# Kernel tuning notes

Measured on AMD Instinct MI355X. Metric: run time of the kernel, lower is better.

## Reference

```python
import jax, jax.numpy as jnp
import numpy as np

B, S, D, H = 4, 1024, 1024, 16
DK = D // H


def _linear_params(key, scale):
    kw, kb = jax.random.split(key)
    W = jax.random.normal(kw, (D, D), dtype=jnp.float32) * scale
    b = jax.random.normal(kb, (D,), dtype=jnp.float32) * 0.01
    return W, b


def setup_inputs() -> dict:
    key = jax.random.key(0)
    ks = jax.random.split(key, 12)
    scale = 1.0 / np.sqrt(D)
    inp = {
        "query": jax.random.normal(ks[0], (B, S, D), dtype=jnp.float32),
        "key": jax.random.normal(ks[1], (B, S, D), dtype=jnp.float32),
        "value": jax.random.normal(ks[2], (B, S, D), dtype=jnp.float32),
        "time_k": jax.random.normal(ks[3], (B, S, D), dtype=jnp.float32),
        "time_v": jax.random.normal(ks[4], (B, S, D), dtype=jnp.float32),
        "mask": jnp.zeros((B, 1, S, S), dtype=jnp.float32),
    }
    names = ["Wq", "bq", "Wk", "bk", "Wv", "bv", "Wtk", "btk", "Wtv", "btv", "Wm", "bm"]
    for i in range(6):
        W, b = _linear_params(ks[5 + i], scale)
        inp[names[2 * i]] = W
        inp[names[2 * i + 1]] = b
    return inp


def _split_heads(x):
    # [B,S,D] -> [B,H,S,DK]
    b, s, _ = x.shape
    return x.reshape(b, s, H, DK).transpose(0, 2, 1, 3)


def reference(query, key, value, time_k, time_v, mask,
              Wq, bq, Wk, bk, Wv, bv, Wtk, btk, Wtv, btv, Wm, bm):
    q = _split_heads(query @ Wq + bq)
    k = _split_heads(key @ Wk + bk)
    v = _split_heads(value @ Wv + bv)
    t_k = _split_heads(time_k @ Wtk + btk)
    t_v = _split_heads(time_v @ Wtv + btv)

    # scores[b,h,i,j] = q_i . k_j + t_k_i . q_j  (note second term uses q on the key axis)
    scores = jnp.einsum("bhid,bhjd->bhij", q, k) + jnp.einsum("bhid,bhjd->bhij", t_k, q)
    # module divides by sqrt(d_model) (query.size(-1)), not sqrt(d_k)
    scores = scores / jnp.sqrt(jnp.float32(D)) + mask
    probs = jax.nn.softmax(scores, axis=-1)

    # dropout is identity (p=0 / eval); squeeze(-2) is a no-op for S>1
    context = jnp.einsum("bhij,bhjd->bhid", probs, v) + jnp.einsum("bhij,bhjd->bhid", probs, t_v)
    x = context.transpose(0, 2, 1, 3).reshape(query.shape[0], -1, D)
    return x @ Wm + bm
```

## Files before the change

### kernel.cpp

```cpp
#include <hip/hip_runtime.h>
#include <hip/hip_bf16.h>
#include <cstdint>
#include <cstddef>

typedef __bf16 bf16;
typedef bf16 bf16x8 __attribute__((ext_vector_type(8)));
typedef bf16 bf16x4 __attribute__((ext_vector_type(4)));
typedef float f32x4 __attribute__((ext_vector_type(4)));
typedef unsigned int u32;

#define DEV static __device__ __forceinline__

DEV f32x4 mfma16(bf16x8 a, bf16x8 b, f32x4 c) {
    return __builtin_amdgcn_mfma_f32_16x16x32_bf16(a, b, c, 0, 0, 0);
}

DEV f32x4 shflx4(f32x4 v, int m) {
    f32x4 r;
    for (int i = 0; i < 4; ++i) r[i] = __shfl_xor(v[i], m, 64);
    return r;
}

DEV bf16x8 cvt8(const float* p) {
    float4 f0 = *(const float4*)p;
    float4 f1 = *(const float4*)(p + 4);
    bf16x8 v;
    v[0] = (bf16)f0.x; v[1] = (bf16)f0.y; v[2] = (bf16)f0.z; v[3] = (bf16)f0.w;
    v[4] = (bf16)f1.x; v[5] = (bf16)f1.y; v[6] = (bf16)f1.z; v[7] = (bf16)f1.w;
    return v;
}

DEV void glo(const bf16* g, bf16* l) {
    __builtin_amdgcn_global_load_lds(
        (const __attribute__((address_space(1))) u32*)g,
        (__attribute__((address_space(3))) u32*)l,
        16, 0, 0);
}


struct PrepArgs {
    const float* w[6];
    const float* act[5];
    bf16* wt;
    bf16* actbf[5];
};

__global__ __launch_bounds__(256) void prep_kernel(PrepArgs p)
{
    const int z = blockIdx.z;
    const int t = threadIdx.x;
    if (z < 6) {
        __shared__ bf16 tile[64][72];
        const float* src = p.w[z];
        bf16* out = p.wt + (size_t)z * 1024 * 1024;
        const int r = t >> 3, c8 = (t & 7) * 8;
        const int row0 = blockIdx.y * 64, col0 = blockIdx.x * 64;
        *(bf16x8*)&tile[r][c8]      = cvt8(&src[(size_t)(row0 + r) * 1024 + col0 + c8]);
        *(bf16x8*)&tile[r + 32][c8] = cvt8(&src[(size_t)(row0 + r + 32) * 1024 + col0 + c8]);
        __syncthreads();
        for (int half = 0; half < 2; ++half) {
            int rr = r + half * 32;
            bf16x8 v;
            for (int j = 0; j < 8; ++j) v[j] = tile[c8 + j][rr];
            *(bf16x8*)&out[(size_t)(col0 + rr) * 1024 + row0 + c8] = v;
        }
    } else {
        const float* src = p.act[z - 6];
        bf16* dst = p.actbf[z - 6];
        const size_t chunk = (size_t)(blockIdx.y * 16 + blockIdx.x) * 16384;
        for (int c = 0; c < 8; ++c) {
            const size_t off = chunk + (size_t)c * 2048 + (size_t)t * 8;
            *(bf16x8*)&dst[off] = cvt8(&src[off]);
        }
    }
}

__global__ __launch_bounds__(256) void maskprep_kernel(
    const float* __restrict__ mask, bf16* __restrict__ maskR)
{
    const int jt = blockIdx.x, it = blockIdx.y, b = blockIdx.z;
    __shared__ bf16 Mt[128 * 72];
    const int t = threadIdx.x, lane = t & 63, w = t >> 6;
    const int ln = lane & 15, qd = lane >> 4;
    {
        const int il = t >> 1, jh = (t & 1) * 32;
        const float* src = &mask[((size_t)b * 1024 + it * 128 + il) * 1024 + jt * 64 + jh];
        *(bf16x8*)&Mt[il * 72 + jh]      = cvt8(src);
        *(bf16x8*)&Mt[il * 72 + jh + 8]  = cvt8(src + 8);
        *(bf16x8*)&Mt[il * 72 + jh + 16] = cvt8(src + 16);
        *(bf16x8*)&Mt[il * 72 + jh + 24] = cvt8(src + 24);
    }
    __syncthreads();
    bf16 m[32];
    for (int si = 0; si < 2; ++si)
        for (int jc = 0; jc < 4; ++jc)
            for (int r = 0; r < 4; ++r) {
                const int il = w * 32 + si * 16 + qd * 4 + r;
                const int jl = jc * 16 + ln;
                m[(si * 4 + jc) * 4 + r] = Mt[il * 72 + jl];
            }
    bf16* dst = &maskR[((((size_t)b * 8 + it) * 16 + jt) * 256 + t) * 32];
    for (int c = 0; c < 4; ++c)
        *(bf16x8*)&dst[c * 8] = *(const bf16x8*)&m[c * 8];
}

struct ProjArgs {
    const bf16* A[5];
    const bf16* W[5];
    const float* bias[5];
    bf16* out[5];
    int vst[5];
};

__global__ __launch_bounds__(256) void proj_gemm(ProjArgs pa)
{
    const int z = blockIdx.z;
    const bf16* A = pa.A[z];
    const bf16* W = pa.W[z];
    const int m0 = blockIdx.x * 128, n0 = blockIdx.y * 128;
    __shared__ bf16 As[128 * 64];
    __shared__ bf16 Bs[128 * 64];
    const int t = threadIdx.x, lane = t & 63, w = t >> 6;
    const int ln = lane & 15, qd = lane >> 4;
    const int wm0 = (w >> 1) * 64, wn0 = (w & 1) * 64;
    const int sub0 = w * 4;
    const int rr = lane >> 3;
    const int cbs = (((lane & 7) ^ rr)) * 8;
    const int lx = ln & 7;
    f32x4 acc[4][4];
    for (int i = 0; i < 4; ++i)
        for (int j = 0; j < 4; ++j)
            acc[i][j] = (f32x4){0.f, 0.f, 0.f, 0.f};
    for (int ks = 0; ks < 16; ++ks) {
        const int bk = ks * 64;
        __syncthreads();
        for (int i = 0; i < 4; ++i) {
            const int row = (sub0 + i) * 8 + rr;
            glo(&W[(size_t)(n0 + row) * 1024 + bk + cbs], &Bs[(sub0 + i) * 512]);
            glo(&A[(size_t)(m0 + row) * 1024 + bk + cbs], &As[(sub0 + i) * 512]);
        }
        __syncthreads();
        for (int kc = 0; kc < 2; ++kc) {
            const int sg = ((kc * 4 + qd) ^ lx) * 8;
            bf16x8 af[4], bfr[4];
            for (int mi = 0; mi < 4; ++mi)
                af[mi] = *(const bf16x8*)&As[(wm0 + mi * 16 + ln) * 64 + sg];
            for (int ni = 0; ni < 4; ++ni)
                bfr[ni] = *(const bf16x8*)&Bs[(wn0 + ni * 16 + ln) * 64 + sg];
            for (int mi = 0; mi < 4; ++mi)
                for (int ni = 0; ni < 4; ++ni)
                    acc[mi][ni] = mfma16(af[mi], bfr[ni], acc[mi][ni]);
        }
    }
    const float* bias = pa.bias[z];
    bf16* out = pa.out[z];
    const int vst = pa.vst[z];
    for (int ni = 0; ni < 4; ++ni) {
        const int n = n0 + wn0 + ni * 16 + ln;
        const float bv = bias[n];
        for (int mi = 0; mi < 4; ++mi) {
            const int mbase = m0 + wm0 + mi * 16 + qd * 4;
            f32x4 v = acc[mi][ni];
            if (vst) {
                const int b = mbase >> 10, s = mbase & 1023;
                bf16x4 pk;
                for (int r = 0; r < 4; ++r) pk[r] = (bf16)(v[r] + bv);
                *(bf16x4*)&out[((size_t)(b * 1024 + n)) * 1024 + s] = pk;
            } else {
                for (int r = 0; r < 4; ++r)
                    out[(size_t)(mbase + r) * 1024 + n] = (bf16)(v[r] + bv);
            }
        }
    }
}

__global__ __launch_bounds__(256) void attn6_kernel(
    const bf16* __restrict__ Qb, const bf16* __restrict__ Kb, const bf16* __restrict__ TKb,
    const bf16* __restrict__ Va, const bf16* __restrict__ Vb,
    const bf16* __restrict__ maskR, bf16* __restrict__ ctx)
{
    const int h = blockIdx.x, it = blockIdx.y, b = blockIdx.z;
    const int i0 = it * 128;
    __shared__ bf16 Ks[64 * 64];
    __shared__ bf16 QJs[64 * 64];
    __shared__ bf16 Vs[64 * 68];
    __shared__ bf16 Ps[128][68];
    const int t = threadIdx.x, lane = t & 63, w = t >> 6;
    const int ln = lane & 15, qd = lane >> 4;
    const int lx = ln & 7;
    const size_t baseQ = ((size_t)b * 1024) * 1024 + (size_t)h * 64;

    bf16x8 qf[2][2], tkf[2][2];
    for (int si = 0; si < 2; ++si) {
        const size_t row = (size_t)(i0 + w * 32 + si * 16 + ln);
        for (int kc = 0; kc < 2; ++kc) {
            qf[si][kc]  = *(const bf16x8*)&Qb [baseQ + row * 1024 + kc * 32 + qd * 8];
            tkf[si][kc] = *(const bf16x8*)&TKb[baseQ + row * 1024 + kc * 32 + qd * 8];
        }
    }

    f32x4 O[2][4];
    f32x4 psum[2];
    for (int si = 0; si < 2; ++si) {
        psum[si] = (f32x4){0.f, 0.f, 0.f, 0.f};
        for (int dc = 0; dc < 4; ++dc) O[si][dc] = (f32x4){0.f, 0.f, 0.f, 0.f};
    }

    const float c1 = 0.045084439f;
    const float c2 = 1.442695041f;

    const size_t mtile0 = (((size_t)b * 8 + it) * 16) * 256 + t;

    for (int jt = 0; jt < 16; ++jt) {
        const int j0 = jt * 64;
        __syncthreads();
        {
            const int rr = lane >> 3;
            const int cbs = ((lane & 7) ^ rr) * 8;
            for (int i = 0; i < 4; ++i) {
                const int u = w * 4 + i;
                if (u < 8) {
                    glo(&Kb[baseQ + (size_t)(j0 + u * 8 + rr) * 1024 + cbs], &Ks[u * 512]);
                } else {
                    const int s = u - 8;
                    glo(&Qb[baseQ + (size_t)(j0 + s * 8 + rr) * 1024 + cbs], &QJs[s * 512]);
                }
            }
        }
        {
            const int vrow = t >> 2, vcol = (t & 3) * 16;
            const size_t va = ((size_t)b * 1024 + h * 64 + vrow) * 1024 + j0 + vcol;
            bf16x8 a0 = *(const bf16x8*)&Va[va];
            bf16x8 a1 = *(const bf16x8*)&Va[va + 8];
            bf16x8 b0 = *(const bf16x8*)&Vb[va];
            bf16x8 b1 = *(const bf16x8*)&Vb[va + 8];
            bf16 s[16];
            for (int e = 0; e < 8; ++e) {
                s[e]     = (bf16)((float)a0[e] + (float)b0[e]);
                s[8 + e] = (bf16)((float)a1[e] + (float)b1[e]);
            }
            bf16* dst = &Vs[vrow * 68 + vcol];
            for (int c = 0; c < 4; ++c)
                *(bf16x4*)&dst[c * 4] = *(const bf16x4*)&s[c * 4];
        }
        bf16x8 mm[4];
        {
            const bf16* mb = &maskR[(mtile0 + (size_t)jt * 256) * 32];
            for (int c = 0; c < 4; ++c) mm[c] = *(const bf16x8*)&mb[c * 8];
        }
        __syncthreads();

        f32x4 sc[2][4];
        for (int jc = 0; jc < 4; ++jc) {
            bf16x8 kf[2], qjf[2];
            for (int kc = 0; kc < 2; ++kc) {
                const int sg = ((kc * 4 + qd) ^ lx) * 8;
                kf[kc]  = *(const bf16x8*)&Ks [(jc * 16 + ln) * 64 + sg];
                qjf[kc] = *(const bf16x8*)&QJs[(jc * 16 + ln) * 64 + sg];
            }
            for (int si = 0; si < 2; ++si) {
                f32x4 a = (f32x4){0.f, 0.f, 0.f, 0.f};
                a = mfma16(qf[si][0], kf[0], a);
                a = mfma16(qf[si][1], kf[1], a);
                a = mfma16(tkf[si][0], qjf[0], a);
                a = mfma16(tkf[si][1], qjf[1], a);
                sc[si][jc] = a;
            }
        }
        for (int si = 0; si < 2; ++si) {
            const int ibl = w * 32 + si * 16 + qd * 4;
            for (int jc = 0; jc < 4; ++jc) {
                const int jl = jc * 16 + ln;
                const int e = si * 4 + jc;
                for (int r = 0; r < 4; ++r) {
                    const float mval = (float)mm[e >> 1][(e & 1) * 4 + r];
                    const float p = exp2f(fmaf(sc[si][jc][r], c1, mval * c2));
                    psum[si][r] += p;
                    Ps[ibl + r][jl] = (bf16)p;
                }
            }
        }
        for (int kc = 0; kc < 2; ++kc) {
            bf16x8 pa[2], vb[4];
            for (int si = 0; si < 2; ++si) {
                bf16x4 lo = *(const bf16x4*)&Ps[w * 32 + si * 16 + ln][kc * 32 + qd * 8];
                bf16x4 hi = *(const bf16x4*)&Ps[w * 32 + si * 16 + ln][kc * 32 + qd * 8 + 4];
                for (int e = 0; e < 4; ++e) { pa[si][e] = lo[e]; pa[si][4 + e] = hi[e]; }
            }
            for (int dc = 0; dc < 4; ++dc) {
                bf16x4 lo = *(const bf16x4*)&Vs[(dc * 16 + ln) * 68 + kc * 32 + qd * 8];
                bf16x4 hi = *(const bf16x4*)&Vs[(dc * 16 + ln) * 68 + kc * 32 + qd * 8 + 4];
                for (int e = 0; e < 4; ++e) { vb[dc][e] = lo[e]; vb[dc][4 + e] = hi[e]; }
            }
            for (int si = 0; si < 2; ++si)
                for (int dc = 0; dc < 4; ++dc)
                    O[si][dc] = mfma16(pa[si], vb[dc], O[si][dc]);
        }
    }

    for (int si = 0; si < 2; ++si) {
        for (int m = 1; m <= 8; m <<= 1) psum[si] += shflx4(psum[si], m);
        f32x4 rl;
        for (int r = 0; r < 4; ++r) rl[r] = 1.0f / psum[si][r];
        const int ibase = i0 + w * 32 + si * 16 + qd * 4;
        for (int dc = 0; dc < 4; ++dc) {
            const int d = h * 64 + dc * 16 + ln;
            f32x4 v = O[si][dc] * rl;
            for (int r = 0; r < 4; ++r)
                ctx[((size_t)b * 1024 + ibase + r) * 1024 + d] = (bf16)v[r];
        }
    }
}

__global__ __launch_bounds__(256) void out_gemm(
    const bf16* __restrict__ A, const bf16* __restrict__ W,
    const float* __restrict__ bias, float* __restrict__ out)
{
    const int m0 = blockIdx.x * 64, n0 = blockIdx.y * 128;
    __shared__ bf16 As[64 * 64];
    __shared__ bf16 Bs[128 * 64];
    const int t = threadIdx.x, lane = t & 63, w = t >> 6;
    const int ln = lane & 15, qd = lane >> 4;
    const int wn0 = w * 32;
    const int rr = lane >> 3;
    const int cbs = ((lane & 7) ^ rr) * 8;
    const int lx = ln & 7;
    f32x4 acc[4][2];
    for (int i = 0; i < 4; ++i)
        for (int j = 0; j < 2; ++j)
            acc[i][j] = (f32x4){0.f, 0.f, 0.f, 0.f};
    for (int ks = 0; ks < 16; ++ks) {
        const int bk = ks * 64;
        __syncthreads();
        for (int i = 0; i < 6; ++i) {
            const int u = w * 6 + i;
            if (u < 8) {
                glo(&A[(size_t)(m0 + u * 8 + rr) * 1024 + bk + cbs], &As[u * 512]);
            } else {
                const int sub = u - 8;
                glo(&W[(size_t)(n0 + sub * 8 + rr) * 1024 + bk + cbs], &Bs[sub * 512]);
            }
        }
        __syncthreads();
        for (int kc = 0; kc < 2; ++kc) {
            const int sg = ((kc * 4 + qd) ^ lx) * 8;
            bf16x8 af[4], bfr[2];
            for (int mi = 0; mi < 4; ++mi)
                af[mi] = *(const bf16x8*)&As[(mi * 16 + ln) * 64 + sg];
            for (int ni = 0; ni < 2; ++ni)
                bfr[ni] = *(const bf16x8*)&Bs[(wn0 + ni * 16 + ln) * 64 + sg];
            for (int mi = 0; mi < 4; ++mi)
                for (int ni = 0; ni < 2; ++ni)
                    acc[mi][ni] = mfma16(af[mi], bfr[ni], acc[mi][ni]);
        }
    }
    for (int ni = 0; ni < 2; ++ni) {
        const int n = n0 + wn0 + ni * 16 + ln;
        const float bv = bias[n];
        for (int mi = 0; mi < 4; ++mi) {
            const int mbase = m0 + mi * 16 + qd * 4;
            f32x4 v = acc[mi][ni];
            for (int r = 0; r < 4; ++r)
                out[(size_t)(mbase + r) * 1024 + n] = v[r] + bv;
        }
    }
}

extern "C" void kernel_launch(void* const* d_in, const int* in_sizes, int n_in,
                              void* d_out, int out_size, void* d_ws, size_t ws_size,
                              hipStream_t stream)
{
    (void)in_sizes; (void)n_in; (void)out_size; (void)ws_size;
    const float* query  = (const float*)d_in[0];
    const float* key    = (const float*)d_in[1];
    const float* value  = (const float*)d_in[2];
    const float* time_k = (const float*)d_in[3];
    const float* time_v = (const float*)d_in[4];
    const float* mask   = (const float*)d_in[5];
    const float* Wq  = (const float*)d_in[6];  const float* bq  = (const float*)d_in[7];
    const float* Wk  = (const float*)d_in[8];  const float* bk  = (const float*)d_in[9];
    const float* Wv  = (const float*)d_in[10]; const float* bv  = (const float*)d_in[11];
    const float* Wtk = (const float*)d_in[12]; const float* btk = (const float*)d_in[13];
    const float* Wtv = (const float*)d_in[14]; const float* btv = (const float*)d_in[15];
    const float* Wm  = (const float*)d_in[16]; const float* bm  = (const float*)d_in[17];

    bf16* ws = (bf16*)d_ws;
    const size_t MM = (size_t)1024 * 1024;
    bf16* WT    = ws;
    bf16* qbf   = ws + 6 * MM;
    bf16* kbf   = ws + 10 * MM;
    bf16* vbf   = ws + 14 * MM;
    bf16* tkbf  = ws + 18 * MM;
    bf16* tvbf  = ws + 22 * MM;
    bf16* Qb    = ws + 26 * MM;
    bf16* Kb    = ws + 30 * MM;
    bf16* TKb   = ws + 34 * MM;
    bf16* VsTa  = ws + 38 * MM;
    bf16* VsTb  = ws + 42 * MM;
    bf16* ctx   = ws + 6 * MM;
    bf16* maskR = (bf16*)d_out;

    PrepArgs pp;
    pp.w[0] = Wq; pp.w[1] = Wk; pp.w[2] = Wv; pp.w[3] = Wtk; pp.w[4] = Wtv; pp.w[5] = Wm;
    pp.wt = WT;
    pp.act[0] = query; pp.act[1] = key; pp.act[2] = value;
    pp.act[3] = time_k; pp.act[4] = time_v;
    pp.actbf[0] = qbf; pp.actbf[1] = kbf; pp.actbf[2] = vbf;
    pp.actbf[3] = tkbf; pp.actbf[4] = tvbf;
    prep_kernel<<<dim3(16, 16, 11), 256, 0, stream>>>(pp);
    maskprep_kernel<<<dim3(16, 8, 4), 256, 0, stream>>>(mask, maskR);

    ProjArgs pa;
    pa.A[0] = qbf;  pa.W[0] = WT + 0 * MM; pa.bias[0] = bq;  pa.out[0] = Qb;   pa.vst[0] = 0;
    pa.A[1] = kbf;  pa.W[1] = WT + 1 * MM; pa.bias[1] = bk;  pa.out[1] = Kb;   pa.vst[1] = 0;
    pa.A[2] = tkbf; pa.W[2] = WT + 3 * MM; pa.bias[2] = btk; pa.out[2] = TKb;  pa.vst[2] = 0;
    pa.A[3] = vbf;  pa.W[3] = WT + 2 * MM; pa.bias[3] = bv;  pa.out[3] = VsTa; pa.vst[3] = 1;
    pa.A[4] = tvbf; pa.W[4] = WT + 4 * MM; pa.bias[4] = btv; pa.out[4] = VsTb; pa.vst[4] = 1;
    proj_gemm<<<dim3(32, 8, 5), 256, 0, stream>>>(pa);

    attn6_kernel<<<dim3(16, 8, 4), 256, 0, stream>>>(
        Qb, Kb, TKb, VsTa, VsTb, maskR, ctx);
    out_gemm<<<dim3(64, 8), 256, 0, stream>>>(ctx, WT + 5 * MM, bm, (float*)d_out);
}
```

Measured before the change: 323.4 us.

## Multi-stage software-pipeline projection GEMM with 4-buffer LDS ring and raw waitcnt barriers

The projection GEMM loop is restructured from a single-buffer load-sync-compute loop with 64-wide K tiles into a 4-slot LDS ring of 32-wide K tiles, keeping three tiles of async global-to-LDS loads in flight while computing the current one. Synchronisation uses explicit s_waitcnt vmcnt plus s_barrier instead of double __syncthreads, the LDS swizzle is reworked for the narrower rows, and MFMA issue is wrapped in s_setprio. The intent is to hide global load latency behind MFMA work. It costs more barriers per K step, and the correctness of the fixed vmcnt counts depends on the exact number of loads issued per stage.

```diff
diff --git a/kernel.cpp b/kernel.cpp
--- a/kernel.cpp
+++ b/kernel.cpp
@@ -36,7 +36,6 @@
         (__attribute__((address_space(3))) u32*)l,
         16, 0, 0);
 }
-
 
 struct PrepArgs {
     const float* w[6];
@@ -112,46 +111,81 @@
     int vst[5];
 };
 
+#define WAITB(n) asm volatile("s_waitcnt vmcnt(" #n ")\n\ts_barrier" ::: "memory")
+
 __global__ __launch_bounds__(256) void proj_gemm(ProjArgs pa)
 {
     const int z = blockIdx.z;
     const bf16* A = pa.A[z];
     const bf16* W = pa.W[z];
     const int m0 = blockIdx.x * 128, n0 = blockIdx.y * 128;
-    __shared__ bf16 As[128 * 64];
-    __shared__ bf16 Bs[128 * 64];
+    __shared__ bf16 As[4 * 128 * 32];
+    __shared__ bf16 Bs[4 * 128 * 32];
     const int t = threadIdx.x, lane = t & 63, w = t >> 6;
     const int ln = lane & 15, qd = lane >> 4;
     const int wm0 = (w >> 1) * 64, wn0 = (w & 1) * 64;
-    const int sub0 = w * 4;
-    const int rr = lane >> 3;
-    const int cbs = (((lane & 7) ^ rr)) * 8;
-    const int lx = ln & 7;
+    const int srow16 = lane >> 2;
+    const int sseg   = lane & 3;
+
     f32x4 acc[4][4];
     for (int i = 0; i < 4; ++i)
         for (int j = 0; j < 4; ++j)
             acc[i][j] = (f32x4){0.f, 0.f, 0.f, 0.f};
-    for (int ks = 0; ks < 16; ++ks) {
-        const int bk = ks * 64;
-        __syncthreads();
-        for (int i = 0; i < 4; ++i) {
-            const int row = (sub0 + i) * 8 + rr;
-            glo(&W[(size_t)(n0 + row) * 1024 + bk + cbs], &Bs[(sub0 + i) * 512]);
-            glo(&A[(size_t)(m0 + row) * 1024 + bk + cbs], &As[(sub0 + i) * 512]);
-        }
-        __syncthreads();
-        for (int kc = 0; kc < 2; ++kc) {
-            const int sg = ((kc * 4 + qd) ^ lx) * 8;
-            bf16x8 af[4], bfr[4];
-            for (int mi = 0; mi < 4; ++mi)
-                af[mi] = *(const bf16x8*)&As[(wm0 + mi * 16 + ln) * 64 + sg];
-            for (int ni = 0; ni < 4; ++ni)
-                bfr[ni] = *(const bf16x8*)&Bs[(wn0 + ni * 16 + ln) * 64 + sg];
-            for (int mi = 0; mi < 4; ++mi)
-                for (int ni = 0; ni < 4; ++ni)
-                    acc[mi][ni] = mfma16(af[mi], bfr[ni], acc[mi][ni]);
-        }
-    }
+
+#define STAGE_TILE(tt_) do {                                                   \
+        const int _tt = (tt_);                                                 \
+        const int _b = _tt & 3;                                                \
+        const int _bk = _tt * 32;                                              \
+        for (int _r = 0; _r < 2; ++_r) {                                       \
+            const int _rows0 = _r * 64 + w * 16;                               \
+            const int _row = _rows0 + srow16;                                  \
+            const int _cs = (sseg ^ ((_row >> 1) & 3)) * 8;                    \
+            glo(&A[(size_t)(m0 + _row) * 1024 + _bk + _cs],                    \
+                &As[_b * 4096 + _rows0 * 32]);                                 \
+            glo(&W[(size_t)(n0 + _row) * 1024 + _bk + _cs],                    \
+                &Bs[_b * 4096 + _rows0 * 32]);                                 \
+        }                                                                      \
+    } while (0)
+
+#define COMPUTE_TILE(tt_) do {                                                 \
+        const int _b = (tt_) & 3;                                              \
+        bf16x8 _af[4], _bf[4];                                                 \
+        for (int _mi = 0; _mi < 4; ++_mi) {                                    \
+            const int _row = wm0 + _mi * 16 + ln;                              \
+            _af[_mi] = *(const bf16x8*)&As[_b * 4096 + _row * 32 +             \
+                                           ((qd ^ ((_row >> 1) & 3)) * 8)];    \
+        }                                                                      \
+        for (int _ni = 0; _ni < 4; ++_ni) {                                    \
+            const int _row = wn0 + _ni * 16 + ln;                              \
+            _bf[_ni] = *(const bf16x8*)&Bs[_b * 4096 + _row * 32 +             \
+                                           ((qd ^ ((_row >> 1) & 3)) * 8)];    \
+        }                                                                      \
+        __builtin_amdgcn_s_setprio(1);                                         \
+        for (int _mi = 0; _mi < 4; ++_mi)                                      \
+            for (int _ni = 0; _ni < 4; ++_ni)                                  \
+                acc[_mi][_ni] = mfma16(_af[_mi], _bf[_ni], acc[_mi][_ni]);     \
+        __builtin_amdgcn_s_setprio(0);                                         \
+    } while (0)
+
+    STAGE_TILE(0);
+    STAGE_TILE(1);
+    STAGE_TILE(2);
+    WAITB(8);
+
+    for (int tt = 0; tt < 29; ++tt) {
+        STAGE_TILE(tt + 3);
+        COMPUTE_TILE(tt);
+        WAITB(8);
+    }
+    COMPUTE_TILE(29);
+    WAITB(4);
+    COMPUTE_TILE(30);
+    WAITB(0);
+    COMPUTE_TILE(31);
+
+#undef STAGE_TILE
+#undef COMPUTE_TILE
+
     const float* bias = pa.bias[z];
     bf16* out = pa.out[z];
     const int vst = pa.vst[z];
```

Measured after the change: 331.8 us. +2.6%, slower.

## Fuse V and time_v projections into one K=2048 GEMM, read V directly

Applied to the files above, without the earlier changes.

Concatenates value|time_v activations and Wv|Wtv weights along K so a single GEMM produces v+t_v with the summed bias. The attention kernel no longer loads two V tensors and adds them into shared memory; it reads MFMA B-fragments of the summed V straight from global memory. This removes one V tensor write and read plus the LDS staging and add, but the z=3 projection blocks now do twice the K work, which creates load imbalance across the grid, and the direct global V loads may be less coalesced than the LDS path.

```diff
diff --git a/kernel.cpp b/kernel.cpp
--- a/kernel.cpp
+++ b/kernel.cpp
@@ -37,12 +37,11 @@
         16, 0, 0);
 }
 
-
 struct PrepArgs {
     const float* w[6];
     const float* act[5];
-    bf16* wt;
-    bf16* actbf[5];
+    bf16* wdst[6];  int wstride[6];
+    bf16* adst[5];  int astride[5];
 };
 
 __global__ __launch_bounds__(256) void prep_kernel(PrepArgs p)
@@ -52,7 +51,8 @@
     if (z < 6) {
         __shared__ bf16 tile[64][72];
         const float* src = p.w[z];
-        bf16* out = p.wt + (size_t)z * 1024 * 1024;
+        bf16* out = p.wdst[z];
+        const int os = p.wstride[z];
         const int r = t >> 3, c8 = (t & 7) * 8;
         const int row0 = blockIdx.y * 64, col0 = blockIdx.x * 64;
         *(bf16x8*)&tile[r][c8]      = cvt8(&src[(size_t)(row0 + r) * 1024 + col0 + c8]);
@@ -62,15 +62,17 @@
             int rr = r + half * 32;
             bf16x8 v;
             for (int j = 0; j < 8; ++j) v[j] = tile[c8 + j][rr];
-            *(bf16x8*)&out[(size_t)(col0 + rr) * 1024 + row0 + c8] = v;
+            *(bf16x8*)&out[(size_t)(col0 + rr) * os + row0 + c8] = v;
         }
     } else {
         const float* src = p.act[z - 6];
-        bf16* dst = p.actbf[z - 6];
+        bf16* dst = p.adst[z - 6];
+        const int as = p.astride[z - 6];
         const size_t chunk = (size_t)(blockIdx.y * 16 + blockIdx.x) * 16384;
         for (int c = 0; c < 8; ++c) {
             const size_t off = chunk + (size_t)c * 2048 + (size_t)t * 8;
-            *(bf16x8*)&dst[off] = cvt8(&src[off]);
+            const size_t row = off >> 10, col = off & 1023;
+            *(bf16x8*)&dst[row * (size_t)as + col] = cvt8(&src[off]);
         }
     }
 }
@@ -105,11 +107,13 @@
 }
 
 struct ProjArgs {
-    const bf16* A[5];
-    const bf16* W[5];
-    const float* bias[5];
-    bf16* out[5];
-    int vst[5];
+    const bf16* A[4];
+    const bf16* W[4];
+    const float* bias[4];
+    const float* bias2[4];
+    bf16* out[4];
+    int vst[4];
+    int nk[4];
 };
 
 __global__ __launch_bounds__(256) void proj_gemm(ProjArgs pa)
@@ -117,6 +121,8 @@
     const int z = blockIdx.z;
     const bf16* A = pa.A[z];
     const bf16* W = pa.W[z];
+    const int nk = pa.nk[z];
+    const int lda = nk << 6;
     const int m0 = blockIdx.x * 128, n0 = blockIdx.y * 128;
     __shared__ bf16 As[128 * 64];
     __shared__ bf16 Bs[128 * 64];
@@ -131,13 +137,13 @@
     for (int i = 0; i < 4; ++i)
         for (int j = 0; j < 4; ++j)
             acc[i][j] = (f32x4){0.f, 0.f, 0.f, 0.f};
-    for (int ks = 0; ks < 16; ++ks) {
+    for (int ks = 0; ks < nk; ++ks) {
         const int bk = ks * 64;
         __syncthreads();
         for (int i = 0; i < 4; ++i) {
             const int row = (sub0 + i) * 8 + rr;
-            glo(&W[(size_t)(n0 + row) * 1024 + bk + cbs], &Bs[(sub0 + i) * 512]);
-            glo(&A[(size_t)(m0 + row) * 1024 + bk + cbs], &As[(sub0 + i) * 512]);
+            glo(&W[(size_t)(n0 + row) * lda + bk + cbs], &Bs[(sub0 + i) * 512]);
+            glo(&A[(size_t)(m0 + row) * lda + bk + cbs], &As[(sub0 + i) * 512]);
         }
         __syncthreads();
         for (int kc = 0; kc < 2; ++kc) {
@@ -153,11 +159,12 @@
         }
     }
     const float* bias = pa.bias[z];
+    const float* bias2 = pa.bias2[z];
     bf16* out = pa.out[z];
     const int vst = pa.vst[z];
     for (int ni = 0; ni < 4; ++ni) {
         const int n = n0 + wn0 + ni * 16 + ln;
-        const float bv = bias[n];
+        const float bv = bias[n] + (bias2 ? bias2[n] : 0.0f);
         for (int mi = 0; mi < 4; ++mi) {
             const int mbase = m0 + wm0 + mi * 16 + qd * 4;
             f32x4 v = acc[mi][ni];
@@ -176,19 +183,19 @@
 
 __global__ __launch_bounds__(256) void attn6_kernel(
     const bf16* __restrict__ Qb, const bf16* __restrict__ Kb, const bf16* __restrict__ TKb,
-    const bf16* __restrict__ Va, const bf16* __restrict__ Vb,
+    const bf16* __restrict__ Vsum,
     const bf16* __restrict__ maskR, bf16* __restrict__ ctx)
 {
     const int h = blockIdx.x, it = blockIdx.y, b = blockIdx.z;
     const int i0 = it * 128;
     __shared__ bf16 Ks[64 * 64];
     __shared__ bf16 QJs[64 * 64];
-    __shared__ bf16 Vs[64 * 68];
     __shared__ bf16 Ps[128][68];
     const int t = threadIdx.x, lane = t & 63, w = t >> 6;
     const int ln = lane & 15, qd = lane >> 4;
     const int lx = ln & 7;
     const size_t baseQ = ((size_t)b * 1024) * 1024 + (size_t)h * 64;
+    const size_t baseV = ((size_t)b * 1024 + h * 64) * 1024;
 
     bf16x8 qf[2][2], tkf[2][2];
     for (int si = 0; si < 2; ++si) {
@@ -227,22 +234,6 @@
                 }
             }
         }
-        {
-            const int vrow = t >> 2, vcol = (t & 3) * 16;
-            const size_t va = ((size_t)b * 1024 + h * 64 + vrow) * 1024 + j0 + vcol;
-            bf16x8 a0 = *(const bf16x8*)&Va[va];
-            bf16x8 a1 = *(const bf16x8*)&Va[va + 8];
-            bf16x8 b0 = *(const bf16x8*)&Vb[va];
-            bf16x8 b1 = *(const bf16x8*)&Vb[va + 8];
-            bf16 s[16];
-            for (int e = 0; e < 8; ++e) {
-                s[e]     = (bf16)((float)a0[e] + (float)b0[e]);
-                s[8 + e] = (bf16)((float)a1[e] + (float)b1[e]);
-            }
-            bf16* dst = &Vs[vrow * 68 + vcol];
-            for (int c = 0; c < 4; ++c)
-                *(bf16x4*)&dst[c * 4] = *(const bf16x4*)&s[c * 4];
-        }
         bf16x8 mm[4];
         {
             const bf16* mb = &maskR[(mtile0 + (size_t)jt * 256) * 32];
@@ -287,11 +278,9 @@
                 bf16x4 hi = *(const bf16x4*)&Ps[w * 32 + si * 16 + ln][kc * 32 + qd * 8 + 4];
                 for (int e = 0; e < 4; ++e) { pa[si][e] = lo[e]; pa[si][4 + e] = hi[e]; }
             }
-            for (int dc = 0; dc < 4; ++dc) {
-                bf16x4 lo = *(const bf16x4*)&Vs[(dc * 16 + ln) * 68 + kc * 32 + qd * 8];
-                bf16x4 hi = *(const bf16x4*)&Vs[(dc * 16 + ln) * 68 + kc * 32 + qd * 8 + 4];
-                for (int e = 0; e < 4; ++e) { vb[dc][e] = lo[e]; vb[dc][4 + e] = hi[e]; }
-            }
+            for (int dc = 0; dc < 4; ++dc)
+                vb[dc] = *(const bf16x8*)&Vsum[baseV + (size_t)(dc * 16 + ln) * 1024
+                                               + j0 + kc * 32 + qd * 8];
             for (int si = 0; si < 2; ++si)
                 for (int dc = 0; dc < 4; ++dc)
                     O[si][dc] = mfma16(pa[si], vb[dc], O[si][dc]);
@@ -386,39 +375,49 @@
 
     bf16* ws = (bf16*)d_ws;
     const size_t MM = (size_t)1024 * 1024;
-    bf16* WT    = ws;
-    bf16* qbf   = ws + 6 * MM;
-    bf16* kbf   = ws + 10 * MM;
-    bf16* vbf   = ws + 14 * MM;
-    bf16* tkbf  = ws + 18 * MM;
-    bf16* tvbf  = ws + 22 * MM;
-    bf16* Qb    = ws + 26 * MM;
-    bf16* Kb    = ws + 30 * MM;
-    bf16* TKb   = ws + 34 * MM;
-    bf16* VsTa  = ws + 38 * MM;
-    bf16* VsTb  = ws + 42 * MM;
-    bf16* ctx   = ws + 6 * MM;
+    bf16* WTq  = ws + 0 * MM;
+    bf16* WTk  = ws + 1 * MM;
+    bf16* WTtk = ws + 2 * MM;
+    bf16* WTm  = ws + 3 * MM;
+    bf16* WT5  = ws + 4 * MM;
+    bf16* qbf  = ws + 6 * MM;
+    bf16* kbf  = ws + 10 * MM;
+    bf16* tkbf = ws + 14 * MM;
+    bf16* A5   = ws + 18 * MM;
+    bf16* Qb   = ws + 26 * MM;
+    bf16* Kb   = ws + 30 * MM;
+    bf16* TKb  = ws + 34 * MM;
+    bf16* VsT  = ws + 38 * MM;
+    bf16* ctx  = ws + 6 * MM;
     bf16* maskR = (bf16*)d_out;
 
     PrepArgs pp;
-    pp.w[0] = Wq; pp.w[1] = Wk; pp.w[2] = Wv; pp.w[3] = Wtk; pp.w[4] = Wtv; pp.w[5] = Wm;
-    pp.wt = WT;
-    pp.act[0] = query; pp.act[1] = key; pp.act[2] = value;
-    pp.act[3] = time_k; pp.act[4] = time_v;
-    pp.actbf[0] = qbf; pp.actbf[1] = kbf; pp.actbf[2] = vbf;
-    pp.actbf[3] = tkbf; pp.actbf[4] = tvbf;
+    pp.w[0] = Wq;  pp.wdst[0] = WTq;        pp.wstride[0] = 1024;
+    pp.w[1] = Wk;  pp.wdst[1] = WTk;        pp.wstride[1] = 1024;
+    pp.w[2] = Wv;  pp.wdst[2] = WT5;        pp.wstride[2] = 2048;
+    pp.w[3] = Wtk; pp.wdst[3] = WTtk;       pp.wstride[3] = 1024;
+    pp.w[4] = Wtv; pp.wdst[4] = WT5 + 1024; pp.wstride[4] = 2048;
+    pp.w[5] = Wm;  pp.wdst[5] = WTm;        pp.wstride[5] = 1024;
+    pp.act[0] = query;  pp.adst[0] = qbf;       pp.astride[0] = 1024;
+    pp.act[1] = key;    pp.adst[1] = kbf;       pp.astride[1] = 1024;
+    pp.act[2] = value;  pp.adst[2] = A5;        pp.astride[2] = 2048;
+    pp.act[3] = time_k; pp.adst[3] = tkbf;      pp.astride[3] = 1024;
+    pp.act[4] = time_v; pp.adst[4] = A5 + 1024; pp.astride[4] = 2048;
     prep_kernel<<<dim3(16, 16, 11), 256, 0, stream>>>(pp);
     maskprep_kernel<<<dim3(16, 8, 4), 256, 0, stream>>>(mask, maskR);
 
     ProjArgs pa;
-    pa.A[0] = qbf;  pa.W[0] = WT + 0 * MM; pa.bias[0] = bq;  pa.out[0] = Qb;   pa.vst[0] = 0;
-    pa.A[1] = kbf;  pa.W[1] = WT + 1 * MM; pa.bias[1] = bk;  pa.out[1] = Kb;   pa.vst[1] = 0;
-    pa.A[2] = tkbf; pa.W[2] = WT + 3 * MM; pa.bias[2] = btk; pa.out[2] = TKb;  pa.vst[2] = 0;
-    pa.A[3] = vbf;  pa.W[3] = WT + 2 * MM; pa.bias[3] = bv;  pa.out[3] = VsTa; pa.vst[3] = 1;
-    pa.A[4] = tvbf; pa.W[4] = WT + 4 * MM; pa.bias[4] = btv; pa.out[4] = VsTb; pa.vst[4] = 1;
-    proj_gemm<<<dim3(32, 8, 5), 256, 0, stream>>>(pa);
+    pa.A[0] = qbf;  pa.W[0] = WTq;  pa.bias[0] = bq;  pa.bias2[0] = nullptr;
+    pa.out[0] = Qb;  pa.vst[0] = 0; pa.nk[0] = 16;
+    pa.A[1] = kbf;  pa.W[1] = WTk;  pa.bias[1] = bk;  pa.bias2[1] = nullptr;
+    pa.out[1] = Kb;  pa.vst[1] = 0; pa.nk[1] = 16;
+    pa.A[2] = tkbf; pa.W[2] = WTtk; pa.bias[2] = btk; pa.bias2[2] = nullptr;
+    pa.out[2] = TKb; pa.vst[2] = 0; pa.nk[2] = 16;
+    pa.A[3] = A5;   pa.W[3] = WT5;  pa.bias[3] = bv;  pa.bias2[3] = btv;
+    pa.out[3] = VsT; pa.vst[3] = 1; pa.nk[3] = 32;
+    proj_gemm<<<dim3(32, 8, 4), 256, 0, stream>>>(pa);
 
     attn6_kernel<<<dim3(16, 8, 4), 256, 0, stream>>>(
-        Qb, Kb, TKb, VsTa, VsTb, maskR, ctx);
-    out_gemm<<<dim3(64, 8), 256, 0, stream>>>(ctx, WT + 5 * MM, bm, (float*)d_out);
-}
+        Qb, Kb, TKb, VsT, maskR, ctx);
+    out_gemm<<<dim3(64, 8), 256, 0, stream>>>(ctx, WTm, bm, (float*)d_out);
+}
```

Measured after the change: 328.3 us. Within noise of the previous version (+1.5%).
